# Performance work log

Hardware: AMD Instinct MI355X
Metric: run time of the kernel (lower is better)

The kernel has to match this reference:

```python
import jax, jax.numpy as jnp
import numpy as np

N, K, D = 65536, 1024, 512


def setup_inputs() -> dict:
    key = jax.random.key(0)
    kx, kc, kv, kp = jax.random.split(key, 4)
    X = jax.random.normal(kx, (N, D), dtype=jnp.float32)
    center = jax.random.normal(kc, (K, D), dtype=jnp.float32)
    var = jax.random.uniform(kv, (K,), dtype=jnp.float32)
    pr = jax.random.uniform(kp, (K,), dtype=jnp.float32)
    threshold = jnp.zeros((1,), dtype=jnp.float32)
    return {"X": X, "center": center, "var": var, "pr": pr, "threshold": threshold}


def reference(X, center, var, pr, threshold):
    # Pairwise squared distances [N, K] via the expanded form
    # avoids materializing the N x K x D tensor).
    x_sq = jnp.sum(X * X, axis=-1, keepdims=True)            # [N, 1]
    c_sq = jnp.sum(center * center, axis=-1)                  # [K]
    cross = jnp.einsum('nd,kd->nk', X, center)                # [N, K]
    sqdist = x_sq - 2.0 * cross + c_sq[None, :]               # [N, K]
    # density: reciprocal-distance weighted sum with weights pr * var
    density = jnp.reciprocal(sqdist) @ (pr * var)             # [N]
    return density - threshold                                 # [N] (threshold [1] broadcasts)
```

## Files before the change

kernel.cpp:

```cpp
#include <hip/hip_runtime.h>
#include <stdint.h>


#define NR 65536
#define KC 1024
#define DD 512

#define BM 256
#define BN 256
#define BK 32
#define NKT (DD / BK)
#define NPART (KC / BN)

#define SLOT_SZ 32768
#define PART_OFF 131072
#define LDS_TOTAL (PART_OFF + 4096)

typedef __bf16 bf16;
typedef __attribute__((ext_vector_type(4))) __bf16 bf16x4;
typedef __attribute__((ext_vector_type(8))) __bf16 bf16x8;
typedef __attribute__((ext_vector_type(4))) float f32x4;

__device__ __forceinline__ void gload16(const void* g, void* l) {
  __builtin_amdgcn_global_load_lds(
      (const __attribute__((address_space(1))) unsigned int*)g,
      (__attribute__((address_space(3))) unsigned int*)l, 16, 0, 0);
}

__global__ __launch_bounds__(256) void prep_kernel(
    const float* __restrict__ X, const float* __restrict__ C,
    const float* __restrict__ var, const float* __restrict__ pr,
    bf16* __restrict__ Xb, bf16* __restrict__ Cb,
    float* __restrict__ xsq, float* __restrict__ csq, float* __restrict__ w) {
  const int row  = (int)((blockIdx.x * 256 + threadIdx.x) >> 6);
  const int lane = (int)(threadIdx.x & 63);
  const bool isX = row < NR;
  const float* srow = isX ? (X + (size_t)row * DD) : (C + (size_t)(row - NR) * DD);
  bf16* drow = isX ? (Xb + (size_t)row * DD) : (Cb + (size_t)(row - NR) * DD);

  float4 a = reinterpret_cast<const float4*>(srow)[lane];
  float4 b = reinterpret_cast<const float4*>(srow)[64 + lane];
  float s = a.x * a.x + a.y * a.y + a.z * a.z + a.w * a.w +
            b.x * b.x + b.y * b.y + b.z * b.z + b.w * b.w;
#pragma unroll
  for (int off = 1; off < 64; off <<= 1) s += __shfl_xor(s, off, 64);

  bf16x4 va = {(bf16)a.x, (bf16)a.y, (bf16)a.z, (bf16)a.w};
  bf16x4 vb = {(bf16)b.x, (bf16)b.y, (bf16)b.z, (bf16)b.w};
  reinterpret_cast<bf16x4*>(drow)[lane]      = va;
  reinterpret_cast<bf16x4*>(drow)[64 + lane] = vb;

  if (lane == 0) {
    if (isX) {
      xsq[row] = s;
    } else {
      const int k = row - NR;
      csq[k] = s;
      w[k]   = pr[k] * var[k];
    }
  }
}


#define STAGE(tn, slotW)                                                        \
  gload16(aSrc0 + (tn) * 32,                 smem + (slotW) + wid * 1024);      \
  gload16(aSrc0 + (size_t)128 * DD + (tn) * 32,                                 \
          smem + (slotW) + 8192 + wid * 1024);                                  \
  gload16(bSrc0 + (tn) * 32,                 smem + (slotW) + 16384 + wid * 1024);\
  gload16(bSrc0 + (size_t)128 * DD + (tn) * 32,                                 \
          smem + (slotW) + 24576 + wid * 1024);

__global__ __launch_bounds__(512, 2) void density_kernel(
    const bf16* __restrict__ Xb, const bf16* __restrict__ Cb,
    const float* __restrict__ xsq, const float* __restrict__ csq,
    const float* __restrict__ w, float* __restrict__ partial) {
  extern __shared__ char smem[];

  const int tid  = (int)threadIdx.x;
  const int lane = tid & 63;
  const int wid  = tid >> 6;
  const int wr   = wid >> 2;
  const int wcn  = wid & 3;
  const int lr   = lane & 15;
  const int lc   = lane >> 4;

  const int bid   = (int)blockIdx.x;
  const int swz   = (bid & 7) * 128 + (bid >> 3);
  const int ntile = swz >> 8;
  const int mtile = swz & 255;
  const int rowBase = mtile * BM;
  const int colBase = ntile * BN;

  const int chunkSw = (((lane & 3) ^ ((lane >> 3) & 3)) << 3);
  const bf16* aSrc0 = Xb + (size_t)(rowBase + wid * 16 + (lane >> 2)) * DD + chunkSw;
  const bf16* bSrc0 = Cb + (size_t)(colBase + wid * 16 + (lane >> 2)) * DD + chunkSw;

  const int rdSw = ((lc ^ ((lr >> 1) & 3)) << 4);
  const int aRd  = (wr * 128 + lr) * 64 + rdSw;
  const int bRd  = 16384 + (wcn * 64 + lr) * 64 + rdSw;

  f32x4 acc[8][4];
#pragma unroll
  for (int m = 0; m < 8; ++m)
#pragma unroll
    for (int n = 0; n < 4; ++n) acc[m][n] = (f32x4){0.f, 0.f, 0.f, 0.f};

  STAGE(0, 0);
  STAGE(1, SLOT_SZ);
  STAGE(2, 2 * SLOT_SZ);
  asm volatile("s_waitcnt vmcnt(8)" ::: "memory");
  __builtin_amdgcn_s_barrier();

#pragma unroll 1
  for (int t = 0; t < NKT; ++t) {
    const int slotR = (t & 3) << 15;

    if (t + 3 < NKT) {
      const int slotW = ((t + 3) & 3) << 15;
      STAGE(t + 3, slotW);
    }

    bf16x8 bg[4];
#pragma unroll
    for (int n = 0; n < 4; ++n)
      bg[n] = *(const bf16x8*)(smem + slotR + bRd + n * 1024);

    __builtin_amdgcn_s_setprio(1);
#pragma unroll
    for (int mi = 0; mi < 8; ++mi) {
      const bf16x8 a = *(const bf16x8*)(smem + slotR + aRd + mi * 1024);
#pragma unroll
      for (int n = 0; n < 4; ++n)
        acc[mi][n] = __builtin_amdgcn_mfma_f32_16x16x32_bf16(
            a, bg[n], acc[mi][n], 0, 0, 0);
    }
    __builtin_amdgcn_s_setprio(0);

    if (t < NKT - 1) {
      if (t < NKT - 3) {
        asm volatile("s_waitcnt vmcnt(8)" ::: "memory");
      } else if (t == NKT - 3) {
        asm volatile("s_waitcnt vmcnt(4)" ::: "memory");
      } else {
        asm volatile("s_waitcnt vmcnt(0)" ::: "memory");
      }
      __builtin_amdgcn_s_barrier();
    }
  }

  float xr[8][4];
#pragma unroll
  for (int m = 0; m < 8; ++m)
#pragma unroll
    for (int j = 0; j < 4; ++j)
      xr[m][j] = xsq[rowBase + wr * 128 + m * 16 + lc * 4 + j];

  float rsum[8][4];
#pragma unroll
  for (int m = 0; m < 8; ++m)
#pragma unroll
    for (int j = 0; j < 4; ++j) rsum[m][j] = 0.f;

#pragma unroll
  for (int n = 0; n < 4; ++n) {
    const int gc = colBase + wcn * 64 + n * 16 + lr;
    const float cs = csq[gc];
    const float ww = w[gc];
#pragma unroll
    for (int m = 0; m < 8; ++m)
#pragma unroll
      for (int j = 0; j < 4; ++j) {
        const float sq = xr[m][j] + cs - 2.f * acc[m][n][j];
        rsum[m][j] += ww * __builtin_amdgcn_rcpf(sq);
      }
  }
#pragma unroll
  for (int m = 0; m < 8; ++m)
#pragma unroll
    for (int j = 0; j < 4; ++j) {
      float v = rsum[m][j];
      v += __shfl_xor(v, 1, 64);
      v += __shfl_xor(v, 2, 64);
      v += __shfl_xor(v, 4, 64);
      v += __shfl_xor(v, 8, 64);
      rsum[m][j] = v;
    }

  float* part = (float*)(smem + PART_OFF);
  __syncthreads();
  if (lr == 0) {
#pragma unroll
    for (int m = 0; m < 8; ++m)
#pragma unroll
      for (int j = 0; j < 4; ++j)
        part[wcn * 256 + wr * 128 + m * 16 + lc * 4 + j] = rsum[m][j];
  }
  __syncthreads();
  if (tid < BM) {
    const float s = part[tid] + part[256 + tid] + part[512 + tid] + part[768 + tid];
    partial[(size_t)ntile * NR + rowBase + tid] = s;
  }
}

__global__ __launch_bounds__(256) void reduce_kernel(
    const float* __restrict__ partial, const float* __restrict__ thr,
    float* __restrict__ out) {
  const int n = (int)(blockIdx.x * 256 + threadIdx.x);
  float s = 0.f;
#pragma unroll
  for (int g = 0; g < NPART; ++g) s += partial[(size_t)g * NR + n];
  out[n] = s - thr[0];
}

extern "C" void kernel_launch(void* const* d_in, const int* in_sizes, int n_in,
                              void* d_out, int out_size, void* d_ws, size_t ws_size,
                              hipStream_t stream) {
  const float* X   = (const float*)d_in[0];
  const float* C   = (const float*)d_in[1];
  const float* var = (const float*)d_in[2];
  const float* pr  = (const float*)d_in[3];
  const float* thr = (const float*)d_in[4];
  float* out = (float*)d_out;

  char* ws = (char*)d_ws;
  bf16* Xb   = (bf16*)(ws);
  bf16* Cb   = (bf16*)(ws + (size_t)NR * DD * 2);
  float* xsq = (float*)(ws + (size_t)NR * DD * 2 + (size_t)KC * DD * 2);
  float* csq = xsq + NR;
  float* w   = csq + KC;
  float* partial = w + KC;

  prep_kernel<<<(NR + KC) / 4, 256, 0, stream>>>(X, C, var, pr, Xb, Cb, xsq, csq, w);
  density_kernel<<<(NR / BM) * NPART, 512, LDS_TOTAL, stream>>>(
      Xb, Cb, xsq, csq, w, partial);
  reduce_kernel<<<NR / 256, 256, 0, stream>>>(partial, thr, out);
}
```

Before: 121.4 us.

## Split K-step into two phases interleaving global loads with MFMA clusters

Reduces prefetch depth from three tiles ahead to two, and splits each K-iteration into two halves. Each half reads its A fragments from LDS, issues half of the next tile's global-to-LDS loads, then runs an MFMA cluster separated by extra barriers. The aim is to spread memory issue across compute phases and keep the matrix units busy. The cost is the shallower prefetch and the extra barriers per iteration, which could stall waves.

```diff
diff --git a/kernel.cpp b/kernel.cpp
--- a/kernel.cpp
+++ b/kernel.cpp
@@ -107,43 +107,67 @@
 
   STAGE(0, 0);
   STAGE(1, SLOT_SZ);
-  STAGE(2, 2 * SLOT_SZ);
-  asm volatile("s_waitcnt vmcnt(8)" ::: "memory");
+  asm volatile("s_waitcnt vmcnt(4)" ::: "memory");
   __builtin_amdgcn_s_barrier();
 
 #pragma unroll 1
   for (int t = 0; t < NKT; ++t) {
     const int slotR = (t & 3) << 15;
-
-    if (t + 3 < NKT) {
-      const int slotW = ((t + 3) & 3) << 15;
-      STAGE(t + 3, slotW);
-    }
+    const int slotW = ((t + 2) & 3) << 15;
+    const bool st = (t + 2) < NKT;
 
     bf16x8 bg[4];
 #pragma unroll
     for (int n = 0; n < 4; ++n)
       bg[n] = *(const bf16x8*)(smem + slotR + bRd + n * 1024);
-
+    bf16x8 af0[4];
+#pragma unroll
+    for (int mi = 0; mi < 4; ++mi)
+      af0[mi] = *(const bf16x8*)(smem + slotR + aRd + mi * 1024);
+
+    if (st) {
+      gload16(aSrc0 + (t + 2) * 32, smem + slotW + wid * 1024);
+      gload16(aSrc0 + (size_t)128 * DD + (t + 2) * 32,
+              smem + slotW + 8192 + wid * 1024);
+    }
+
+    __builtin_amdgcn_s_barrier();
+    asm volatile("s_waitcnt lgkmcnt(0)" ::: "memory");
     __builtin_amdgcn_s_setprio(1);
 #pragma unroll
-    for (int mi = 0; mi < 8; ++mi) {
-      const bf16x8 a = *(const bf16x8*)(smem + slotR + aRd + mi * 1024);
+    for (int mi = 0; mi < 4; ++mi)
 #pragma unroll
       for (int n = 0; n < 4; ++n)
         acc[mi][n] = __builtin_amdgcn_mfma_f32_16x16x32_bf16(
-            a, bg[n], acc[mi][n], 0, 0, 0);
-    }
+            af0[mi], bg[n], acc[mi][n], 0, 0, 0);
     __builtin_amdgcn_s_setprio(0);
+    __builtin_amdgcn_s_barrier();
+
+    bf16x8 af1[4];
+#pragma unroll
+    for (int mi = 0; mi < 4; ++mi)
+      af1[mi] = *(const bf16x8*)(smem + slotR + aRd + (4 + mi) * 1024);
+
+    if (st) {
+      gload16(bSrc0 + (t + 2) * 32, smem + slotW + 16384 + wid * 1024);
+      gload16(bSrc0 + (size_t)128 * DD + (t + 2) * 32,
+              smem + slotW + 24576 + wid * 1024);
+    }
+
+    __builtin_amdgcn_s_barrier();
+    asm volatile("s_waitcnt lgkmcnt(0)" ::: "memory");
+    __builtin_amdgcn_s_setprio(1);
+#pragma unroll
+    for (int mi = 0; mi < 4; ++mi)
+#pragma unroll
+      for (int n = 0; n < 4; ++n)
+        acc[4 + mi][n] = __builtin_amdgcn_mfma_f32_16x16x32_bf16(
+            af1[mi], bg[n], acc[4 + mi][n], 0, 0, 0);
+    __builtin_amdgcn_s_setprio(0);
 
     if (t < NKT - 1) {
-      if (t < NKT - 3) {
-        asm volatile("s_waitcnt vmcnt(8)" ::: "memory");
-      } else if (t == NKT - 3) {
-        asm volatile("s_waitcnt vmcnt(4)" ::: "memory");
-      } else {
-        asm volatile("s_waitcnt vmcnt(0)" ::: "memory");
-      }
+      if (st) asm volatile("s_waitcnt vmcnt(4)" ::: "memory");
+      else    asm volatile("s_waitcnt vmcnt(0)" ::: "memory");
       __builtin_amdgcn_s_barrier();
     }
   }
```

Result: no change. 120.9 us (-0.4%).
